# Kernel tuning notes

Measured on AMD Instinct MI355X. Metric: run time of the kernel, lower is better.

The kernel has to match this reference:

```python
import jax, jax.numpy as jnp
import numpy as np

# Spiking time schedule: B_n = (1+0.5)*X_n = 1500 per spiking layer (X_n=1000),
# chained via set_params: layer k has t_min = 1500*k, t_max = 1500*(k+1).
B_N = 1500.0


def _region_idx(H, W):
    # 0=center, 1=TL, 2=top, 3=TR, 4=right, 5=BR, 6=bottom, 7=BL, 8=left
    r = np.zeros((H, W), np.int32)
    r[0, :] = 2; r[-1, :] = 6; r[:, 0] = 8; r[:, -1] = 4
    r[0, 0] = 1; r[0, -1] = 3; r[-1, -1] = 5; r[-1, 0] = 7
    return jnp.asarray(r)


def _im2col3(x, t_min):
    # x: [B,H,W,C] -> patches [B,H,W,9*C]; 'same' pad with value t_min
    B, H, W, C = x.shape
    xp = jnp.pad(x, ((0, 0), (1, 1), (1, 1), (0, 0)), constant_values=t_min)
    cols = [xp[:, dy:dy + H, dx:dx + W, :] for dy in range(3) for dx in range(3)]
    return jnp.concatenate(cols, axis=-1)


def _spiking_conv(x, Wk, D, t_min, t_max):
    # ti = (tj - t_min) @ W + (t_max - t_min - D_region) + t_min, clamped at t_max
    p = _im2col3(x, t_min)                       # [B,H,W,9C]
    lin = jnp.einsum('bhwk,kf->bhwf', p - t_min, Wk)
    Dmap = D[_region_idx(x.shape[1], x.shape[2])]  # [H,W,F] border-aware thresholds
    return jnp.minimum(lin + (t_max - Dmap), t_max)


def _spiking_dense(x, Wk, D, t_min, t_max):
    return jnp.minimum((x - t_min) @ Wk + (t_max - D), t_max)


def _pool2(x):
    B, H, W, C = x.shape
    return x.reshape(B, H // 2, 2, W // 2, 2, C).max(axis=(2, 4))


def _forward(x, Wc1, Dc1, Wc2, Dc2, Wc3, Dc3, Wc4, Dc4, Wd1, Dd1, Wout, Dout):
    x = _spiking_conv(x, Wc1, Dc1, 0.0, 1500.0)
    x = _spiking_conv(x, Wc2, Dc2, 1500.0, 3000.0)
    x = _pool2(x)
    x = _spiking_conv(x, Wc3, Dc3, 3000.0, 4500.0)
    x = _spiking_conv(x, Wc4, Dc4, 4500.0, 6000.0)
    x = _pool2(x)
    x = x.reshape(x.shape[0], -1)                 # [B, 16*16*128]
    x = _spiking_dense(x, Wd1, Dd1, 6000.0, 7500.0)
    # output layer: alpha*(t_min - t_min_prev) + (t_min - tj)@W == D_i + (t_min - tj)@W
    return Dout + (7500.0 - x) @ Wout


def setup_inputs() -> dict:
    key = jax.random.key(0)
    ks = jax.random.split(key, 14)
    B, H, C0 = 32, 64, 1

    def w(k, fan_in, fan_out):
        return (jax.random.normal(k, (fan_in, fan_out), jnp.float32)
                / np.float32(np.sqrt(fan_in)))

    def d(k, shape):
        return jax.random.uniform(k, shape, jnp.float32) * 10.0

    return {
        'x': jax.random.uniform(ks[0], (B, H, H, C0), jnp.float32),
        'Wc1': w(ks[1], 9 * C0, 64),    'Dc1': d(ks[2], (9, 64)),
        'Wc2': w(ks[3], 9 * 64, 64),    'Dc2': d(ks[4], (9, 64)),
        'Wc3': w(ks[5], 9 * 64, 128),   'Dc3': d(ks[6], (9, 128)),
        'Wc4': w(ks[7], 9 * 128, 128),  'Dc4': d(ks[8], (9, 128)),
        'Wd1': w(ks[9], 16 * 16 * 128, 256), 'Dd1': d(ks[10], (256,)),
        'Wout': w(ks[11], 256, 10),     'Dout': d(ks[12], (10,)),
    }


def reference(x, Wc1, Dc1, Wc2, Dc2, Wc3, Dc3, Wc4, Dc4, Wd1, Dd1, Wout, Dout):
    return _forward(x, Wc1, Dc1, Wc2, Dc2, Wc3, Dc3, Wc4, Dc4, Wd1, Dd1, Wout, Dout)
```

## Files before the change

kernel.cpp:

```cpp
#include <hip/hip_runtime.h>
#include <hip/hip_bf16.h>

#define DEVINL __device__ __forceinline__

typedef __attribute__((ext_vector_type(8)))  short short8;
typedef __attribute__((ext_vector_type(4)))  float float4v;

DEVINL float bf2f(unsigned short u) { return __uint_as_float(((unsigned)u) << 16); }
DEVINL unsigned short f2bf(float f) {
  unsigned u = __float_as_uint(f);
  unsigned r = u + 0x7FFFu + ((u >> 16) & 1u);
  return (unsigned short)(r >> 16);
}

DEVINL int region_of(int h, int w, int n) {
  if (h == 0)     return (w == 0) ? 1 : ((w == n-1) ? 3 : 2);
  if (h == n-1)   return (w == 0) ? 7 : ((w == n-1) ? 5 : 6);
  return (w == 0) ? 8 : ((w == n-1) ? 4 : 0);
}

__global__ void sentinel_k(float* out, float v) {
  int t = blockIdx.x*64 + threadIdx.x;
  if (t < 320) out[t] = v;
}

__global__ void wtrans_all(const float* __restrict__ W2, const float* __restrict__ W3,
                           const float* __restrict__ W4,
                           unsigned short* __restrict__ T2, unsigned short* __restrict__ T3,
                           unsigned short* __restrict__ T4)
{
  int y = blockIdx.y;
  const float* W = (y == 0) ? W2 : (y == 1) ? W3 : W4;
  unsigned short* T = (y == 0) ? T2 : (y == 1) ? T3 : T4;
  int Ksteps = (y == 2) ? 36 : 18;
  int NT = (y == 0) ? 4 : 8;
  int F  = (y == 0) ? 64 : 128;
  int i = blockIdx.x*256 + threadIdx.x;
  if (i >= Ksteps*NT*64) return;
  int lane = i & 63, nt = (i >> 6) % NT, kstep = i / (64*NT);
  int f = nt*16 + (lane & 15);
  int kbase = kstep*32 + (lane >> 4)*8;
  unsigned short v[8];
  #pragma unroll
  for (int j = 0; j < 8; j++) v[j] = f2bf(W[(kbase + j)*F + f]);
  ushort4* q = (ushort4*)&T[(size_t)i * 8];
  q[0] = make_ushort4(v[0], v[1], v[2], v[3]);
  q[1] = make_ushort4(v[4], v[5], v[6], v[7]);
}

__global__ __launch_bounds__(256) void conv1_k(const float* __restrict__ x,
    const float* __restrict__ Wf, const float* __restrict__ Df,
    unsigned short* __restrict__ out)
{
  int h = blockIdx.x, b = blockIdx.y, t = threadIdx.x;
  __shared__ float a[3][66];
  for (int idx = t; idx < 3*66; idx += 256) {
    int dy = idx / 66, wcol = idx % 66;
    int hh = h + dy - 1, w = wcol - 1;
    float v = 0.f;
    if (hh >= 0 && hh < 64 && w >= 0 && w < 64)
      v = x[(b*64 + hh)*64 + w];
    a[dy][wcol] = v;
  }
  __syncthreads();
  int f = t & 63, wq = t >> 6;
  float wk[9];
  #pragma unroll
  for (int k = 0; k < 9; k++) wk[k] = Wf[k*64 + f];
  for (int wi = 0; wi < 16; wi++) {
    int w = wq*16 + wi;
    float acc = 0.f;
    #pragma unroll
    for (int dy = 0; dy < 3; dy++)
      #pragma unroll
      for (int dx = 0; dx < 3; dx++)
        acc += a[dy][w+dx] * wk[dy*3+dx];
    int r = region_of(h, w, 64);
    out[((b*64 + h)*64 + w)*64 + f] = f2bf(fminf(acc - Df[r*64 + f], 0.f));
  }
}

template<int C, int F, int N, bool POOL>
__global__ __launch_bounds__(256) void conv_mfma(
    const unsigned short* __restrict__ U, const unsigned short* __restrict__ Wt,
    const float* __restrict__ Df, unsigned short* __restrict__ out)
{
  constexpr int RC   = POOL ? 2 : 1;
  constexpr int ROWS = RC + 2;
  constexpr int Cpad = C + 8;
  constexpr int NT = F / 16;
  constexpr int MT = N / 16;
  constexpr int WNT = NT / 4;

  __shared__ __align__(16) unsigned short lds[ROWS*(N+2)*Cpad];

  int b = blockIdx.y, hp = blockIdx.x, t = threadIdx.x;
  int h0 = hp * RC;

  const int stage16 = ROWS*(N+2)*(C/8);
  for (int i = t; i < stage16; i += 256) {
    int c8 = i % (C/8), wc = (i/(C/8)) % (N+2), r = i/((C/8)*(N+2));
    int hh = h0 - 1 + r, w = wc - 1;
    float4 v = make_float4(0.f,0.f,0.f,0.f);
    if (hh >= 0 && hh < N && w >= 0 && w < N)
      v = *(const float4*)&U[(((size_t)b*N + hh)*N + w)*C + c8*8];
    *(float4*)&lds[(r*(N+2) + wc)*Cpad + c8*8] = v;
  }
  __syncthreads();

  int lane = t & 63, wave = t >> 6;
  int quad = lane >> 4, lm = lane & 15;

  union ABu { float4 f4; short8 v; };

  float4v acc[RC][MT][WNT];
  #pragma unroll
  for (int hi = 0; hi < RC; hi++)
    #pragma unroll
    for (int m = 0; m < MT; m++)
      #pragma unroll
      for (int n = 0; n < WNT; n++)
        acc[hi][m][n] = (float4v){0.f, 0.f, 0.f, 0.f};

  #pragma unroll
  for (int dy = 0; dy < 3; dy++)
  #pragma unroll
  for (int dx = 0; dx < 3; dx++)
  for (int c0 = 0; c0 < C; c0 += 32) {
    int kstep = (dy*3 + dx)*(C/32) + (c0 >> 5);
    ABu bfr[WNT];
    #pragma unroll
    for (int n = 0; n < WNT; n++)
      bfr[n].f4 = *(const float4*)&Wt[(size_t)((kstep*NT + wave*WNT + n)*64 + lane)*8];
    #pragma unroll
    for (int hi = 0; hi < RC; hi++) {
      ABu afr[MT];
      #pragma unroll
      for (int m = 0; m < MT; m++)
        afr[m].f4 = *(const float4*)&lds[((hi+dy)*(N+2) + (m*16 + lm + dx))*Cpad + c0 + quad*8];
      #pragma unroll
      for (int n = 0; n < WNT; n++)
        #pragma unroll
        for (int m = 0; m < MT; m++)
          acc[hi][m][n] = __builtin_amdgcn_mfma_f32_16x16x32_bf16(afr[m].v, bfr[n].v, acc[hi][m][n], 0, 0, 0);
    }
  }

  if (POOL) {
    constexpr int M2 = N/2;
    #pragma unroll
    for (int m = 0; m < MT; m++)
      #pragma unroll
      for (int n = 0; n < WNT; n++) {
        int f = (wave*WNT + n)*16 + lm;
        #pragma unroll
        for (int rp = 0; rp < 2; rp++) {
          float mx = -1e30f;
          #pragma unroll
          for (int hi = 0; hi < 2; hi++)
            #pragma unroll
            for (int rr = 0; rr < 2; rr++) {
              int h = h0 + hi, w = m*16 + quad*4 + 2*rp + rr;
              float v = fminf(acc[hi][m][n][2*rp+rr] - Df[region_of(h, w, N)*F + f], 0.f);
              mx = fmaxf(mx, v);
            }
          int wp = m*8 + quad*2 + rp;
          out[(((size_t)b*M2 + hp)*M2 + wp)*F + f] = f2bf(mx);
        }
      }
  } else {
    int h = h0;
    #pragma unroll
    for (int m = 0; m < MT; m++)
      #pragma unroll
      for (int n = 0; n < WNT; n++) {
        int f = (wave*WNT + n)*16 + lm;
        #pragma unroll
        for (int r = 0; r < 4; r++) {
          int w = m*16 + quad*4 + r;
          int reg = region_of(h, w, N);
          float v = fminf(acc[0][m][n][r] - Df[reg*F + f], 0.f);
          out[(((size_t)b*N + h)*N + w)*F + f] = f2bf(v);
        }
      }
  }
}

__global__ __launch_bounds__(256) void dense_k(const unsigned short* __restrict__ act,
    const float* __restrict__ W, float* __restrict__ part)
{
  int blk = blockIdx.x, t = threadIdx.x;
  int kblk = blk >> 1, fh = blk & 1;
  int k0 = kblk * 128;
  __shared__ float a[128][36];
  for (int idx = t; idx < 32*128; idx += 256) {
    int bb = idx >> 7, kc = idx & 127;
    a[kc][bb] = bf2f(act[(size_t)bb*32768 + k0 + kc]);
  }
  __syncthreads();
  int f0 = fh*128 + (t & 31)*4, b0 = (t >> 5)*4;
  float acc[4][4] = {};
  for (int kc = 0; kc < 128; kc++) {
    float4 wv = *(const float4*)&W[(size_t)(k0 + kc)*256 + f0];
    #pragma unroll
    for (int bb = 0; bb < 4; bb++) {
      float av = a[kc][b0 + bb];
      acc[bb][0] += av * wv.x;
      acc[bb][1] += av * wv.y;
      acc[bb][2] += av * wv.z;
      acc[bb][3] += av * wv.w;
    }
  }
  #pragma unroll
  for (int bb = 0; bb < 4; bb++) {
    float4 v = make_float4(acc[bb][0], acc[bb][1], acc[bb][2], acc[bb][3]);
    *(float4*)&part[(size_t)kblk*8192 + (b0+bb)*256 + f0] = v;
  }
}

__global__ void reduce_k(const float* __restrict__ part, const float* __restrict__ Dd,
                         float* __restrict__ ud)
{
  int i = blockIdx.x*256 + threadIdx.x;
  float s = 0.f;
  #pragma unroll 4
  for (int blk = 0; blk < 256; blk++) s += part[(size_t)blk*8192 + i];
  ud[i] = fminf(s - Dd[i & 255], 0.f);
}

__global__ void final_k(const float* __restrict__ ud, const float* __restrict__ Wo,
                        const float* __restrict__ Do, float* __restrict__ out)
{
  int t = blockIdx.x*64 + threadIdx.x;
  if (t >= 320) return;
  int b = t / 10, o = t % 10;
  float acc = 0.f;
  for (int f = 0; f < 256; f++) acc += ud[b*256 + f] * Wo[f*10 + o];
  out[t] = Do[o] - acc;
}

extern "C" void kernel_launch(void* const* d_in, const int* in_sizes, int n_in,
                              void* d_out, int out_size, void* d_ws, size_t ws_size,
                              hipStream_t stream)
{
  float* outp = (float*)d_out;

  if (n_in != 13) { sentinel_k<<<5, 64, 0, stream>>>(outp, 200.f); return; }
  const int exp_sz[13] = {131072, 576, 576, 36864, 576, 73728, 1152,
                          147456, 1152, 8388608, 256, 2560, 10};
  for (int i = 0; i < 13; i++)
    if (in_sizes[i] != exp_sz[i]) {
      sentinel_k<<<5, 64, 0, stream>>>(outp, 1000.f + 100.f*i); return;
    }
  if (ws_size < (37u << 20)) { sentinel_k<<<5, 64, 0, stream>>>(outp, 500.f); return; }

  char* wsb = (char*)d_ws;
  const float* x    = (const float*)d_in[0];
  const float* Wc1  = (const float*)d_in[1];
  const float* Dc1  = (const float*)d_in[2];
  const float* Wc2  = (const float*)d_in[3];
  const float* Dc2  = (const float*)d_in[4];
  const float* Wc3  = (const float*)d_in[5];
  const float* Dc3  = (const float*)d_in[6];
  const float* Wc4  = (const float*)d_in[7];
  const float* Dc4  = (const float*)d_in[8];
  const float* Wd1  = (const float*)d_in[9];
  const float* Dd1  = (const float*)d_in[10];
  const float* Wout = (const float*)d_in[11];
  const float* Dout = (const float*)d_in[12];

  float* ud = (float*)wsb;
  unsigned short* Wt2 = (unsigned short*)(wsb + (1u << 20));
  unsigned short* Wt3 = (unsigned short*)(wsb + (1u << 20) + 262144);
  unsigned short* Wt4 = (unsigned short*)(wsb + (1u << 20) + 524288);
  unsigned short* U1 = (unsigned short*)(wsb + (2u  << 20));
  unsigned short* P2 = (unsigned short*)(wsb + (19u << 20));
  unsigned short* U3 = (unsigned short*)(wsb + (2u  << 20));
  unsigned short* P4 = (unsigned short*)(wsb + (19u << 20));
  float* part        = (float*)(wsb + (2u  << 20));

  wtrans_all<<<dim3(72, 3), 256, 0, stream>>>(Wc2, Wc3, Wc4, Wt2, Wt3, Wt4);
  conv1_k<<<dim3(64, 32), 256, 0, stream>>>(x, Wc1, Dc1, U1);
  conv_mfma<64, 64, 64, true><<<dim3(32, 32), 256, 0, stream>>>(U1, Wt2, Dc2, P2);
  conv_mfma<64, 128, 32, false><<<dim3(32, 32), 256, 0, stream>>>(P2, Wt3, Dc3, U3);
  conv_mfma<128, 128, 32, true><<<dim3(16, 32), 256, 0, stream>>>(U3, Wt4, Dc4, P4);
  dense_k<<<512, 256, 0, stream>>>(P4, Wd1, part);
  reduce_k<<<32, 256, 0, stream>>>(part, Dd1, ud);
  final_k<<<5, 64, 0, stream>>>(ud, Wout, Dout, outp);
}
```

Measured before the change: 190.5 us.

## Split conv MFMA waves over M and N, vectorize dense LDS reads, add unrolls

The conv MFMA kernel gains a template parameter that splits the four waves across both the spatial (M) and filter (N) tile dimensions instead of only N. Conv2 uses a 2x2 wave split, so each wave holds fewer accumulators and loads fewer A fragments. The dense kernel now reads four batch activations from LDS with one float4 load. Unroll pragmas are added to the staging, channel, reduce and final loops. Heavier unrolling may raise register pressure and code size.

```diff
diff --git a/kernel.cpp b/kernel.cpp
--- a/kernel.cpp
+++ b/kernel.cpp
@@ -80,7 +80,7 @@
   }
 }
 
-template<int C, int F, int N, bool POOL>
+template<int C, int F, int N, bool POOL, int WSM>
 __global__ __launch_bounds__(256) void conv_mfma(
     const unsigned short* __restrict__ U, const unsigned short* __restrict__ Wt,
     const float* __restrict__ Df, unsigned short* __restrict__ out)
@@ -90,7 +90,9 @@
   constexpr int Cpad = C + 8;
   constexpr int NT = F / 16;
   constexpr int MT = N / 16;
-  constexpr int WNT = NT / 4;
+  constexpr int WSN = 4 / WSM;
+  constexpr int MW = MT / WSM;
+  constexpr int NW = NT / WSN;
 
   __shared__ __align__(16) unsigned short lds[ROWS*(N+2)*Cpad];
 
@@ -98,6 +100,7 @@
   int h0 = hp * RC;
 
   const int stage16 = ROWS*(N+2)*(C/8);
+  #pragma unroll 4
   for (int i = t; i < stage16; i += 256) {
     int c8 = i % (C/8), wc = (i/(C/8)) % (N+2), r = i/((C/8)*(N+2));
     int hh = h0 - 1 + r, w = wc - 1;
@@ -109,50 +112,53 @@
   __syncthreads();
 
   int lane = t & 63, wave = t >> 6;
+  int wm = wave / WSN, wn = wave % WSN;
   int quad = lane >> 4, lm = lane & 15;
 
   union ABu { float4 f4; short8 v; };
 
-  float4v acc[RC][MT][WNT];
+  float4v acc[RC][MW][NW];
   #pragma unroll
   for (int hi = 0; hi < RC; hi++)
     #pragma unroll
-    for (int m = 0; m < MT; m++)
-      #pragma unroll
-      for (int n = 0; n < WNT; n++)
+    for (int m = 0; m < MW; m++)
+      #pragma unroll
+      for (int n = 0; n < NW; n++)
         acc[hi][m][n] = (float4v){0.f, 0.f, 0.f, 0.f};
 
   #pragma unroll
   for (int dy = 0; dy < 3; dy++)
   #pragma unroll
   for (int dx = 0; dx < 3; dx++)
+  #pragma unroll
   for (int c0 = 0; c0 < C; c0 += 32) {
     int kstep = (dy*3 + dx)*(C/32) + (c0 >> 5);
-    ABu bfr[WNT];
-    #pragma unroll
-    for (int n = 0; n < WNT; n++)
-      bfr[n].f4 = *(const float4*)&Wt[(size_t)((kstep*NT + wave*WNT + n)*64 + lane)*8];
+    ABu bfr[NW];
+    #pragma unroll
+    for (int n = 0; n < NW; n++)
+      bfr[n].f4 = *(const float4*)&Wt[(size_t)((kstep*NT + wn*NW + n)*64 + lane)*8];
     #pragma unroll
     for (int hi = 0; hi < RC; hi++) {
-      ABu afr[MT];
-      #pragma unroll
-      for (int m = 0; m < MT; m++)
-        afr[m].f4 = *(const float4*)&lds[((hi+dy)*(N+2) + (m*16 + lm + dx))*Cpad + c0 + quad*8];
-      #pragma unroll
-      for (int n = 0; n < WNT; n++)
+      ABu afr[MW];
+      #pragma unroll
+      for (int m = 0; m < MW; m++)
+        afr[m].f4 = *(const float4*)&lds[((hi+dy)*(N+2) + ((wm*MW + m)*16 + lm + dx))*Cpad + c0 + quad*8];
+      #pragma unroll
+      for (int n = 0; n < NW; n++)
         #pragma unroll
-        for (int m = 0; m < MT; m++)
+        for (int m = 0; m < MW; m++)
           acc[hi][m][n] = __builtin_amdgcn_mfma_f32_16x16x32_bf16(afr[m].v, bfr[n].v, acc[hi][m][n], 0, 0, 0);
     }
   }
 
-  if (POOL) {
+  if constexpr (POOL) {
     constexpr int M2 = N/2;
     #pragma unroll
-    for (int m = 0; m < MT; m++)
-      #pragma unroll
-      for (int n = 0; n < WNT; n++) {
-        int f = (wave*WNT + n)*16 + lm;
+    for (int m = 0; m < MW; m++)
+      #pragma unroll
+      for (int n = 0; n < NW; n++) {
+        int mm = wm*MW + m;
+        int f = (wn*NW + n)*16 + lm;
         #pragma unroll
         for (int rp = 0; rp < 2; rp++) {
           float mx = -1e30f;
@@ -160,24 +166,25 @@
           for (int hi = 0; hi < 2; hi++)
             #pragma unroll
             for (int rr = 0; rr < 2; rr++) {
-              int h = h0 + hi, w = m*16 + quad*4 + 2*rp + rr;
+              int h = h0 + hi, w = mm*16 + quad*4 + 2*rp + rr;
               float v = fminf(acc[hi][m][n][2*rp+rr] - Df[region_of(h, w, N)*F + f], 0.f);
               mx = fmaxf(mx, v);
             }
-          int wp = m*8 + quad*2 + rp;
+          int wp = mm*8 + quad*2 + rp;
           out[(((size_t)b*M2 + hp)*M2 + wp)*F + f] = f2bf(mx);
         }
       }
   } else {
     int h = h0;
     #pragma unroll
-    for (int m = 0; m < MT; m++)
-      #pragma unroll
-      for (int n = 0; n < WNT; n++) {
-        int f = (wave*WNT + n)*16 + lm;
+    for (int m = 0; m < MW; m++)
+      #pragma unroll
+      for (int n = 0; n < NW; n++) {
+        int mm = wm*MW + m;
+        int f = (wn*NW + n)*16 + lm;
         #pragma unroll
         for (int r = 0; r < 4; r++) {
-          int w = m*16 + quad*4 + r;
+          int w = mm*16 + quad*4 + r;
           int reg = region_of(h, w, N);
           float v = fminf(acc[0][m][n][r] - Df[reg*F + f], 0.f);
           out[(((size_t)b*N + h)*N + w)*F + f] = f2bf(v);
@@ -200,15 +207,18 @@
   __syncthreads();
   int f0 = fh*128 + (t & 31)*4, b0 = (t >> 5)*4;
   float acc[4][4] = {};
+  #pragma unroll 8
   for (int kc = 0; kc < 128; kc++) {
     float4 wv = *(const float4*)&W[(size_t)(k0 + kc)*256 + f0];
+    float4 av = *(const float4*)&a[kc][b0];
+    const float* avp = (const float*)&av;
     #pragma unroll
     for (int bb = 0; bb < 4; bb++) {
-      float av = a[kc][b0 + bb];
-      acc[bb][0] += av * wv.x;
-      acc[bb][1] += av * wv.y;
-      acc[bb][2] += av * wv.z;
-      acc[bb][3] += av * wv.w;
+      float avx = avp[bb];
+      acc[bb][0] += avx * wv.x;
+      acc[bb][1] += avx * wv.y;
+      acc[bb][2] += avx * wv.z;
+      acc[bb][3] += avx * wv.w;
     }
   }
   #pragma unroll
@@ -223,7 +233,7 @@
 {
   int i = blockIdx.x*256 + threadIdx.x;
   float s = 0.f;
-  #pragma unroll 4
+  #pragma unroll 16
   for (int blk = 0; blk < 256; blk++) s += part[(size_t)blk*8192 + i];
   ud[i] = fminf(s - Dd[i & 255], 0.f);
 }
@@ -235,6 +245,7 @@
   if (t >= 320) return;
   int b = t / 10, o = t % 10;
   float acc = 0.f;
+  #pragma unroll 8
   for (int f = 0; f < 256; f++) acc += ud[b*256 + f] * Wo[f*10 + o];
   out[t] = Do[o] - acc;
 }
@@ -281,9 +292,9 @@
 
   wtrans_all<<<dim3(72, 3), 256, 0, stream>>>(Wc2, Wc3, Wc4, Wt2, Wt3, Wt4);
   conv1_k<<<dim3(64, 32), 256, 0, stream>>>(x, Wc1, Dc1, U1);
-  conv_mfma<64, 64, 64, true><<<dim3(32, 32), 256, 0, stream>>>(U1, Wt2, Dc2, P2);
-  conv_mfma<64, 128, 32, false><<<dim3(32, 32), 256, 0, stream>>>(P2, Wt3, Dc3, U3);
-  conv_mfma<128, 128, 32, true><<<dim3(16, 32), 256, 0, stream>>>(U3, Wt4, Dc4, P4);
+  conv_mfma<64, 64, 64, true, 2><<<dim3(32, 32), 256, 0, stream>>>(U1, Wt2, Dc2, P2);
+  conv_mfma<64, 128, 32, false, 1><<<dim3(32, 32), 256, 0, stream>>>(P2, Wt3, Dc3, U3);
+  conv_mfma<128, 128, 32, true, 1><<<dim3(16, 32), 256, 0, stream>>>(U3, Wt4, Dc4, P4);
   dense_k<<<512, 256, 0, stream>>>(P4, Wd1, part);
   reduce_k<<<32, 256, 0, stream>>>(part, Dd1, ud);
   final_k<<<5, 64, 0, stream>>>(ud, Wout, Dout, outp);
```

Result: faster. 180.9 us (-5.0%).
